# Kernel optimization log

Measured on AMD Instinct MI355X. Metric: run time of the kernel, lower is better.

## Reference

```python
import jax, jax.numpy as jnp
import numpy as np

DIM = 1024
NUM_HEADS = 16
HEAD_DIM = 64  # DIM // NUM_HEADS
BATCH = 2
SEQ = 2048


def setup_inputs() -> dict:
    key = jax.random.key(0)
    ks = jax.random.split(key, 6)
    x = jax.random.normal(ks[0], (BATCH, SEQ, DIM), dtype=jnp.float32)
    # Linear weights stored as [in, out] so y = x @ W (same math as torch Linear).
    Wq = jax.random.normal(ks[1], (DIM, DIM), dtype=jnp.float32) * (DIM ** -0.5)
    # MQA: single shared KV head of size HEAD_DIM.
    Wk = jax.random.normal(ks[2], (DIM, HEAD_DIM), dtype=jnp.float32) * (DIM ** -0.5)
    Wv = jax.random.normal(ks[3], (DIM, HEAD_DIM), dtype=jnp.float32) * (DIM ** -0.5)
    Wo = jax.random.normal(ks[4], (DIM, DIM), dtype=jnp.float32) * (DIM ** -0.5)
    bo = jax.random.normal(ks[5], (DIM,), dtype=jnp.float32) * 0.01
    return {"x": x, "Wq": Wq, "Wk": Wk, "Wv": Wv, "Wo": Wo, "bo": bo}


def reference(x, Wq, Wk, Wv, Wo, bo):
    b, s, _ = x.shape
    scale = HEAD_DIM ** -0.5
    # Per-head queries [b, h, s, d]
    q = (x @ Wq).reshape(b, s, NUM_HEADS, HEAD_DIM).transpose(0, 2, 1, 3) * scale
    # Shared single KV head [b, s, d]
    k = x @ Wk
    v = x @ Wv
    # Materialized scores [b, h, s_q, s_k]
    scores = jnp.einsum('bhqd,bkd->bhqk', q, k)
    causal = jnp.tril(jnp.ones((s, s), dtype=bool))  # True where allowed
    scores = jnp.where(causal, scores, -jnp.inf)
    # Manual stable softmax (max, exp, sum, div) as in the original
    max_scores = jnp.max(scores, axis=-1, keepdims=True)
    exp_scores = jnp.exp(scores - max_scores)
    attn = exp_scores / jnp.sum(exp_scores, axis=-1, keepdims=True)
    out = jnp.einsum('bhqk,bkd->bhqd', attn, v)  # [b, h, s, d]
    out = out.transpose(0, 2, 1, 3).reshape(b, s, DIM)
    return out @ Wo + bo
```

## Files before the change

### kernel.cpp

```cpp
#include <hip/hip_runtime.h>

typedef unsigned short u16;
typedef __attribute__((ext_vector_type(8))) short short8;
typedef __attribute__((ext_vector_type(4))) float f32x4;

static __device__ __forceinline__ u16 f32_to_bf16(float f) {
  unsigned u = __float_as_uint(f);
  u += 0x7fffu + ((u >> 16) & 1u);
  return (u16)(u >> 16);
}

static __device__ __forceinline__ void async16(u16* lds, const u16* g) {
  __builtin_amdgcn_global_load_lds(
      (const __attribute__((address_space(1))) void*)g,
      (__attribute__((address_space(3))) void*)lds, 16, 0, 0);
}


__global__ void __launch_bounds__(256) prep_kernel(
    const float* __restrict__ x,
    const float* __restrict__ Wq, const float* __restrict__ Wk,
    const float* __restrict__ Wv, const float* __restrict__ Wo,
    u16* __restrict__ Xb, u16* __restrict__ WqT, u16* __restrict__ WkvT,
    u16* __restrict__ WoT) {
  __shared__ u16 T[64][72];
  int id = blockIdx.x;
  int tid = threadIdx.x;
  if (id < 2048) {
    int base = (id * 256 + tid) * 8;
    float4 a = *(const float4*)&x[base];
    float4 b = *(const float4*)&x[base + 4];
    short8 v;
    v[0] = (short)f32_to_bf16(a.x); v[1] = (short)f32_to_bf16(a.y);
    v[2] = (short)f32_to_bf16(a.z); v[3] = (short)f32_to_bf16(a.w);
    v[4] = (short)f32_to_bf16(b.x); v[5] = (short)f32_to_bf16(b.y);
    v[6] = (short)f32_to_bf16(b.z); v[7] = (short)f32_to_bf16(b.w);
    *(short8*)&Xb[base] = v;
    return;
  }
  int id2 = id - 2048;
  const float* src; u16* dst; int tk, tn, src_ld, row_off;
  if (id2 < 256)      { src = Wq; dst = WqT;  tk = id2 & 15; tn = id2 >> 4; src_ld = 1024; row_off = 0; }
  else if (id2 < 512) { int i = id2 - 256; src = Wo; dst = WoT; tk = i & 15; tn = i >> 4; src_ld = 1024; row_off = 0; }
  else if (id2 < 528) { src = Wk; dst = WkvT; tk = id2 - 512; tn = 0; src_ld = 64; row_off = 0; }
  else                { src = Wv; dst = WkvT; tk = id2 - 528; tn = 0; src_ld = 64; row_off = 64; }
  int k0 = tk * 64, n0 = tn * 64;
#pragma unroll
  for (int it = 0; it < 2; ++it) {
    int c = tid + it * 256;
    int r = c >> 3, cc = (c & 7) * 8;
    const float* p = &src[(k0 + r) * src_ld + n0 + cc];
    float4 a = *(const float4*)&p[0];
    float4 b = *(const float4*)&p[4];
    short8 v;
    v[0] = (short)f32_to_bf16(a.x); v[1] = (short)f32_to_bf16(a.y);
    v[2] = (short)f32_to_bf16(a.z); v[3] = (short)f32_to_bf16(a.w);
    v[4] = (short)f32_to_bf16(b.x); v[5] = (short)f32_to_bf16(b.y);
    v[6] = (short)f32_to_bf16(b.z); v[7] = (short)f32_to_bf16(b.w);
    *(short8*)&T[r][cc] = v;
  }
  __syncthreads();
#pragma unroll
  for (int it = 0; it < 2; ++it) {
    int c = tid + it * 256;
    int r = c >> 3, cc = (c & 7) * 8;
    short8 v;
#pragma unroll
    for (int j = 0; j < 8; ++j) v[j] = (short)T[cc + j][r];
    *(short8*)&dst[(row_off + n0 + r) * 1024 + k0 + cc] = v;
  }
}

__device__ __forceinline__ void stage_64x128(
    const u16* __restrict__ A, const u16* __restrict__ BT, int m0, int K,
    int k0, u16* As, u16* Bs, int w, int lrow, int swz8) {
#pragma unroll
  for (int it = 0; it < 2; ++it) {
    int W = w * 2 + it;
    async16(As + W * 512, &A[(size_t)(m0 + W * 8 + lrow) * K + k0 + swz8]);
  }
#pragma unroll
  for (int it = 0; it < 4; ++it) {
    int W = w * 4 + it;
    async16(Bs + W * 512, &BT[(size_t)(W * 8 + lrow) * K + k0 + swz8]);
  }
}

__device__ __forceinline__ void gemm_core_64x128_db(
    const u16* __restrict__ A, const u16* __restrict__ BT, int m0, int K,
    f32x4 (&acc)[2][4], u16* As, u16* Bs,
    int lane, int w, int wr, int wc, int g, int lo) {
  int lrow = lane >> 3;
  int swz8 = ((lane & 7) ^ lrow) * 8;
  int lo7 = lo & 7;
  const int NK = K >> 6;
  stage_64x128(A, BT, m0, K, 0, As, Bs, w, lrow, swz8);
  for (int kt = 0; kt < NK; ++kt) {
    int cur = kt & 1;
    __syncthreads();
    if (kt + 1 < NK)
      stage_64x128(A, BT, m0, K, (kt + 1) * 64,
                   As + (cur ^ 1) * 4096, Bs + (cur ^ 1) * 8192, w, lrow, swz8);
    const u16* Asc = As + cur * 4096;
    const u16* Bsc = Bs + cur * 8192;
#pragma unroll
    for (int ks = 0; ks < 2; ++ks) {
      int pc = ((ks * 4 + g) ^ lo7) * 8;
      short8 af[2], bf[4];
#pragma unroll
      for (int i = 0; i < 2; ++i)
        af[i] = *(const short8*)&Asc[(wr * 32 + i * 16 + lo) * 64 + pc];
#pragma unroll
      for (int i = 0; i < 4; ++i)
        bf[i] = *(const short8*)&Bsc[(wc * 64 + i * 16 + lo) * 64 + pc];
#pragma unroll
      for (int mi = 0; mi < 2; ++mi)
#pragma unroll
        for (int ni = 0; ni < 4; ++ni)
          acc[mi][ni] = __builtin_amdgcn_mfma_f32_16x16x32_bf16(
              af[mi], bf[ni], acc[mi][ni], 0, 0, 0);
    }
  }
}

__global__ void __launch_bounds__(256) qkv_gemm(
    const u16* __restrict__ Xb, const u16* __restrict__ WqT,
    const u16* __restrict__ WkvT, u16* __restrict__ Qb, u16* __restrict__ KVb,
    u16* __restrict__ VTb) {
  __shared__ u16 As[2 * 64 * 64];
  __shared__ u16 Bs[2 * 128 * 64];
  int tid = threadIdx.x, lane = tid & 63, w = tid >> 6;
  int wr = w >> 1, wc = w & 1, g = lane >> 4, lo = lane & 15;
  int m0 = blockIdx.x * 64, nb = blockIdx.y;
  const u16* BT = (nb < 8) ? (WqT + (size_t)nb * 128 * 1024) : WkvT;
  f32x4 acc[2][4];
  f32x4 zz = {0.f, 0.f, 0.f, 0.f};
#pragma unroll
  for (int i = 0; i < 2; ++i)
#pragma unroll
    for (int j = 0; j < 4; ++j) acc[i][j] = zz;
  gemm_core_64x128_db(Xb, BT, m0, 1024, acc, As, Bs, lane, w, wr, wc, g, lo);
#pragma unroll
  for (int mi = 0; mi < 2; ++mi)
#pragma unroll
    for (int ni = 0; ni < 4; ++ni)
#pragma unroll
      for (int r = 0; r < 4; ++r) {
        int row = m0 + wr * 32 + mi * 16 + g * 4 + r;
        int col = wc * 64 + ni * 16 + lo;
        u16 v = f32_to_bf16(acc[mi][ni][r]);
        if (nb < 8) {
          Qb[row * 1024 + nb * 128 + col] = v;
        } else if (wc == 0) {
          KVb[row * 64 + col] = v;
        } else {
          int d = col - 64;
          VTb[(((row >> 11) * 64) + d) * 2048 + (row & 2047)] = v;
        }
      }
}

__global__ void __launch_bounds__(256, 2) attn_kernel(
    const u16* __restrict__ Qb, const u16* __restrict__ KVb,
    const u16* __restrict__ VTb, u16* __restrict__ AOb) {
  __shared__ u16 Ks[2][64 * 64];
  __shared__ u16 Vt[2][64 * 64];
  __shared__ u16 Ps[4][16][72];
  int tid = threadIdx.x, lane = tid & 63, w = tid >> 6;
  int gq = lane >> 4, lo = lane & 15;
  int pg = blockIdx.x;
  int h = blockIdx.y;
  int z = blockIdx.z;
  int b = z;
  int a = z ? (15 - pg) : pg;
  int hi = 31 - a;
  int qb_lo = a * 64 + w * 16;
  int qb_hi = hi * 64 + w * 16;
  int lrow = lane >> 3;
  int swz8 = ((lane & 7) ^ lrow) * 8;
  int lo7 = lo & 7;

  short8 qf_lo[2], qf_hi[2];
  {
    const u16* qp = &Qb[(size_t)(b * 2048 + qb_lo + lo) * 1024 + h * 64];
    qf_lo[0] = *(const short8*)&qp[gq * 8];
    qf_lo[1] = *(const short8*)&qp[32 + gq * 8];
    const u16* qp2 = &Qb[(size_t)(b * 2048 + qb_hi + lo) * 1024 + h * 64];
    qf_hi[0] = *(const short8*)&qp2[gq * 8];
    qf_hi[1] = *(const short8*)&qp2[32 + gq * 8];
  }

  short8 ones;
#pragma unroll
  for (int j = 0; j < 8; ++j) ones[j] = (short)0x3F80;

  f32x4 zz = {0.f, 0.f, 0.f, 0.f};
  f32x4 oacc_lo[4], oacc_hi[4], l_lo, l_hi;
#pragma unroll
  for (int i = 0; i < 4; ++i) { oacc_lo[i] = zz; oacc_hi[i] = zz; }
  l_lo = zz; l_hi = zz;

  const float kExp = 0.18033688011112042f;
  const float kOff = 11.541560327111707f;

  auto do_strip = [&](const short8 (&qf)[2], f32x4 (&oacc)[4], f32x4& l_acc,
                      int qbase, bool diag, int k0,
                      const u16* Kc, const u16* Vc) {
    f32x4 sacc[4];
#pragma unroll
    for (int ns = 0; ns < 4; ++ns) sacc[ns] = zz;
#pragma unroll
    for (int ks = 0; ks < 2; ++ks) {
      int pc = ((ks * 4 + gq) ^ lo7) * 8;
      short8 kf[4];
#pragma unroll
      for (int ns = 0; ns < 4; ++ns)
        kf[ns] = *(const short8*)&Kc[(ns * 16 + lo) * 64 + pc];
#pragma unroll
      for (int ns = 0; ns < 4; ++ns)
        sacc[ns] = __builtin_amdgcn_mfma_f32_16x16x32_bf16(
            qf[ks], kf[ns], sacc[ns], 0, 0, 0);
    }
#pragma unroll
    for (int ns = 0; ns < 4; ++ns)
#pragma unroll
      for (int r = 0; r < 4; ++r) {
        float p = __builtin_amdgcn_exp2f(fmaf(sacc[ns][r], kExp, -kOff));
        if (diag) {
          int qg = qbase + gq * 4 + r;
          int kg = k0 + ns * 16 + lo;
          if (kg > qg) p = 0.f;
        }
        Ps[w][gq * 4 + r][ns * 16 + lo] = (u16)(__float_as_uint(p) >> 16);
      }
    __threadfence_block();
#pragma unroll
    for (int k2 = 0; k2 < 2; ++k2) {
      short8 pf = *(const short8*)&Ps[w][lo][k2 * 32 + gq * 8];
      int pc = ((k2 * 4 + gq) ^ lo7) * 8;
      short8 vf[4];
#pragma unroll
      for (int ds = 0; ds < 4; ++ds)
        vf[ds] = *(const short8*)&Vc[(ds * 16 + lo) * 64 + pc];
#pragma unroll
      for (int ds = 0; ds < 4; ++ds)
        oacc[ds] = __builtin_amdgcn_mfma_f32_16x16x32_bf16(
            pf, vf[ds], oacc[ds], 0, 0, 0);
      l_acc = __builtin_amdgcn_mfma_f32_16x16x32_bf16(pf, ones, l_acc, 0, 0, 0);
    }
  };

  auto stage_kv = [&](int t, int bu) {
#pragma unroll
    for (int it = 0; it < 2; ++it) {
      int W = w * 2 + it;
      async16(&Ks[bu][W * 512],
              &KVb[(size_t)(b * 2048 + t * 64 + W * 8 + lrow) * 64 + swz8]);
      async16(&Vt[bu][W * 512],
              &VTb[((size_t)b * 64 + W * 8 + lrow) * 2048 + t * 64 + swz8]);
    }
  };

  int nst = hi + 1;
  stage_kv(0, 0);
  for (int t = 0; t < nst; ++t) {
    int cur = t & 1;
    __syncthreads();
    if (t + 1 < nst) stage_kv(t + 1, cur ^ 1);
    int k0 = t * 64;
    do_strip(qf_hi, oacc_hi, l_hi, qb_hi, t == hi, k0, Ks[cur], Vt[cur]);
    if (t <= a)
      do_strip(qf_lo, oacc_lo, l_lo, qb_lo, t == a, k0, Ks[cur], Vt[cur]);
  }

#pragma unroll
  for (int r = 0; r < 4; ++r) {
    float inv_lo = 1.0f / l_lo[r];
    float inv_hi = 1.0f / l_hi[r];
    int row_lo = b * 2048 + qb_lo + gq * 4 + r;
    int row_hi = b * 2048 + qb_hi + gq * 4 + r;
#pragma unroll
    for (int ds = 0; ds < 4; ++ds) {
      AOb[row_lo * 1024 + h * 64 + ds * 16 + lo] = f32_to_bf16(oacc_lo[ds][r] * inv_lo);
      AOb[row_hi * 1024 + h * 64 + ds * 16 + lo] = f32_to_bf16(oacc_hi[ds][r] * inv_hi);
    }
  }
}

__global__ void __launch_bounds__(256) out_gemm(
    const u16* __restrict__ A, const u16* __restrict__ WoT,
    const float* __restrict__ bias, float* __restrict__ C) {
  __shared__ u16 As[2 * 64 * 64];
  __shared__ u16 Bs[2 * 128 * 64];
  int tid = threadIdx.x, lane = tid & 63, w = tid >> 6;
  int wr = w >> 1, wc = w & 1, g = lane >> 4, lo = lane & 15;
  int m0 = blockIdx.x * 64, nb = blockIdx.y;
  const u16* BT = WoT + (size_t)nb * 128 * 1024;
  f32x4 acc[2][4];
  f32x4 zz = {0.f, 0.f, 0.f, 0.f};
#pragma unroll
  for (int i = 0; i < 2; ++i)
#pragma unroll
    for (int j = 0; j < 4; ++j) acc[i][j] = zz;
  gemm_core_64x128_db(A, BT, m0, 1024, acc, As, Bs, lane, w, wr, wc, g, lo);
#pragma unroll
  for (int mi = 0; mi < 2; ++mi)
#pragma unroll
    for (int ni = 0; ni < 4; ++ni)
#pragma unroll
      for (int r = 0; r < 4; ++r) {
        int row = m0 + wr * 32 + mi * 16 + g * 4 + r;
        int col = nb * 128 + wc * 64 + ni * 16 + lo;
        C[row * 1024 + col] = acc[mi][ni][r] + bias[col];
      }
}

extern "C" void kernel_launch(void* const* d_in, const int* in_sizes, int n_in,
                              void* d_out, int out_size, void* d_ws, size_t ws_size,
                              hipStream_t stream) {
  const float* x  = (const float*)d_in[0];
  const float* Wq = (const float*)d_in[1];
  const float* Wk = (const float*)d_in[2];
  const float* Wv = (const float*)d_in[3];
  const float* Wo = (const float*)d_in[4];
  const float* bo = (const float*)d_in[5];
  float* out = (float*)d_out;

  u16* ws   = (u16*)d_ws;
  u16* AOb  = ws;
  u16* KVb  = AOb + 4194304;
  u16* VTb  = KVb + 262144;
  u16* Xb   = VTb + 262144;
  u16* WqT  = Xb + 4194304;
  u16* WoT  = WqT + 1048576;
  u16* WkvT = WoT + 1048576;
  u16* Qb   = (u16*)d_out;

  prep_kernel<<<2592, 256, 0, stream>>>(x, Wq, Wk, Wv, Wo, Xb, WqT, WkvT, WoT);
  qkv_gemm<<<dim3(64, 9), 256, 0, stream>>>(Xb, WqT, WkvT, Qb, KVb, VTb);
  attn_kernel<<<dim3(16, 16, 2), 256, 0, stream>>>(Qb, KVb, VTb, AOb);
  out_gemm<<<dim3(64, 8), 256, 0, stream>>>(AOb, WoT, bo, out);
}
```

Baseline: 158.1 us.

## Restructure attention to one query tile per block with transposed MFMA and register row sums

The attention kernel drops the paired low/high query-tile scheme and instead launches one 64-row query tile per block, with a rotated block-to-tile mapping to spread causal work across the grid. The QK and PV MFMAs swap operand order so each lane holds a query column. The row sum is then accumulated in registers and reduced by shuffles, replacing the extra ones-matrix MFMA. P and the output are stored with packed bf16 conversion into a swizzled, unpadded LDS layout, and occupancy is raised to 4 blocks per SM. This removes the extra MFMA and lowers register pressure, but gives up the perfect load balance of pairing tiles and relies on the scheduler to absorb the uneven causal tile lengths.

```diff
diff --git a/kernel.cpp b/kernel.cpp
--- a/kernel.cpp
+++ b/kernel.cpp
@@ -8,6 +8,12 @@
   unsigned u = __float_as_uint(f);
   u += 0x7fffu + ((u >> 16) & 1u);
   return (u16)(u >> 16);
+}
+
+static __device__ __forceinline__ unsigned cvt_pk_bf16(float a, float b) {
+  unsigned r;
+  asm("v_cvt_pk_bf16_f32 %0, %1, %2" : "=v"(r) : "v"(a), "v"(b));
+  return r;
 }
 
 static __device__ __forceinline__ void async16(u16* lds, const u16* g) {
@@ -160,95 +166,37 @@
       }
 }
 
-__global__ void __launch_bounds__(256, 2) attn_kernel(
+__global__ void __launch_bounds__(256, 4) attn_kernel(
     const u16* __restrict__ Qb, const u16* __restrict__ KVb,
     const u16* __restrict__ VTb, u16* __restrict__ AOb) {
   __shared__ u16 Ks[2][64 * 64];
   __shared__ u16 Vt[2][64 * 64];
-  __shared__ u16 Ps[4][16][72];
+  __shared__ u16 Ps[4][16][64];
   int tid = threadIdx.x, lane = tid & 63, w = tid >> 6;
   int gq = lane >> 4, lo = lane & 15;
-  int pg = blockIdx.x;
   int h = blockIdx.y;
-  int z = blockIdx.z;
-  int b = z;
-  int a = z ? (15 - pg) : pg;
-  int hi = 31 - a;
-  int qb_lo = a * 64 + w * 16;
-  int qb_hi = hi * 64 + w * 16;
+  int b = blockIdx.z;
+  int a = (blockIdx.x + (h & 8) + (b << 4)) & 31;
+  int qb = a * 64 + w * 16;
   int lrow = lane >> 3;
   int swz8 = ((lane & 7) ^ lrow) * 8;
   int lo7 = lo & 7;
 
-  short8 qf_lo[2], qf_hi[2];
+  short8 qf[2];
   {
-    const u16* qp = &Qb[(size_t)(b * 2048 + qb_lo + lo) * 1024 + h * 64];
-    qf_lo[0] = *(const short8*)&qp[gq * 8];
-    qf_lo[1] = *(const short8*)&qp[32 + gq * 8];
-    const u16* qp2 = &Qb[(size_t)(b * 2048 + qb_hi + lo) * 1024 + h * 64];
-    qf_hi[0] = *(const short8*)&qp2[gq * 8];
-    qf_hi[1] = *(const short8*)&qp2[32 + gq * 8];
-  }
-
-  short8 ones;
-#pragma unroll
-  for (int j = 0; j < 8; ++j) ones[j] = (short)0x3F80;
+    const u16* qp = &Qb[(size_t)(b * 2048 + qb + lo) * 1024 + h * 64];
+    qf[0] = *(const short8*)&qp[gq * 8];
+    qf[1] = *(const short8*)&qp[32 + gq * 8];
+  }
 
   f32x4 zz = {0.f, 0.f, 0.f, 0.f};
-  f32x4 oacc_lo[4], oacc_hi[4], l_lo, l_hi;
-#pragma unroll
-  for (int i = 0; i < 4; ++i) { oacc_lo[i] = zz; oacc_hi[i] = zz; }
-  l_lo = zz; l_hi = zz;
+  f32x4 oacc[4];
+#pragma unroll
+  for (int i = 0; i < 4; ++i) oacc[i] = zz;
+  float lsum = 0.f;
 
   const float kExp = 0.18033688011112042f;
   const float kOff = 11.541560327111707f;
-
-  auto do_strip = [&](const short8 (&qf)[2], f32x4 (&oacc)[4], f32x4& l_acc,
-                      int qbase, bool diag, int k0,
-                      const u16* Kc, const u16* Vc) {
-    f32x4 sacc[4];
-#pragma unroll
-    for (int ns = 0; ns < 4; ++ns) sacc[ns] = zz;
-#pragma unroll
-    for (int ks = 0; ks < 2; ++ks) {
-      int pc = ((ks * 4 + gq) ^ lo7) * 8;
-      short8 kf[4];
-#pragma unroll
-      for (int ns = 0; ns < 4; ++ns)
-        kf[ns] = *(const short8*)&Kc[(ns * 16 + lo) * 64 + pc];
-#pragma unroll
-      for (int ns = 0; ns < 4; ++ns)
-        sacc[ns] = __builtin_amdgcn_mfma_f32_16x16x32_bf16(
-            qf[ks], kf[ns], sacc[ns], 0, 0, 0);
-    }
-#pragma unroll
-    for (int ns = 0; ns < 4; ++ns)
-#pragma unroll
-      for (int r = 0; r < 4; ++r) {
-        float p = __builtin_amdgcn_exp2f(fmaf(sacc[ns][r], kExp, -kOff));
-        if (diag) {
-          int qg = qbase + gq * 4 + r;
-          int kg = k0 + ns * 16 + lo;
-          if (kg > qg) p = 0.f;
-        }
-        Ps[w][gq * 4 + r][ns * 16 + lo] = (u16)(__float_as_uint(p) >> 16);
-      }
-    __threadfence_block();
-#pragma unroll
-    for (int k2 = 0; k2 < 2; ++k2) {
-      short8 pf = *(const short8*)&Ps[w][lo][k2 * 32 + gq * 8];
-      int pc = ((k2 * 4 + gq) ^ lo7) * 8;
-      short8 vf[4];
-#pragma unroll
-      for (int ds = 0; ds < 4; ++ds)
-        vf[ds] = *(const short8*)&Vc[(ds * 16 + lo) * 64 + pc];
-#pragma unroll
-      for (int ds = 0; ds < 4; ++ds)
-        oacc[ds] = __builtin_amdgcn_mfma_f32_16x16x32_bf16(
-            pf, vf[ds], oacc[ds], 0, 0, 0);
-      l_acc = __builtin_amdgcn_mfma_f32_16x16x32_bf16(pf, ones, l_acc, 0, 0, 0);
-    }
-  };
 
   auto stage_kv = [&](int t, int bu) {
 #pragma unroll
@@ -261,29 +209,79 @@
     }
   };
 
-  int nst = hi + 1;
+  int nst = a + 1;
   stage_kv(0, 0);
   for (int t = 0; t < nst; ++t) {
     int cur = t & 1;
     __syncthreads();
     if (t + 1 < nst) stage_kv(t + 1, cur ^ 1);
-    int k0 = t * 64;
-    do_strip(qf_hi, oacc_hi, l_hi, qb_hi, t == hi, k0, Ks[cur], Vt[cur]);
-    if (t <= a)
-      do_strip(qf_lo, oacc_lo, l_lo, qb_lo, t == a, k0, Ks[cur], Vt[cur]);
-  }
-
-#pragma unroll
-  for (int r = 0; r < 4; ++r) {
-    float inv_lo = 1.0f / l_lo[r];
-    float inv_hi = 1.0f / l_hi[r];
-    int row_lo = b * 2048 + qb_lo + gq * 4 + r;
-    int row_hi = b * 2048 + qb_hi + gq * 4 + r;
-#pragma unroll
-    for (int ds = 0; ds < 4; ++ds) {
-      AOb[row_lo * 1024 + h * 64 + ds * 16 + lo] = f32_to_bf16(oacc_lo[ds][r] * inv_lo);
-      AOb[row_hi * 1024 + h * 64 + ds * 16 + lo] = f32_to_bf16(oacc_hi[ds][r] * inv_hi);
-    }
+    const u16* Kc = Ks[cur];
+    const u16* Vc = Vt[cur];
+
+    f32x4 sacc[4];
+#pragma unroll
+    for (int ns = 0; ns < 4; ++ns) sacc[ns] = zz;
+#pragma unroll
+    for (int ks = 0; ks < 2; ++ks) {
+      int pc = ((ks * 4 + gq) ^ lo7) * 8;
+      short8 kf[4];
+#pragma unroll
+      for (int ns = 0; ns < 4; ++ns)
+        kf[ns] = *(const short8*)&Kc[(ns * 16 + lo) * 64 + pc];
+#pragma unroll
+      for (int ns = 0; ns < 4; ++ns)
+        sacc[ns] = __builtin_amdgcn_mfma_f32_16x16x32_bf16(
+            kf[ns], qf[ks], sacc[ns], 0, 0, 0);
+    }
+
+    bool diag = (t == a);
+    int qg = qb + lo;
+#pragma unroll
+    for (int ns = 0; ns < 4; ++ns) {
+      float p[4];
+#pragma unroll
+      for (int r = 0; r < 4; ++r) {
+        float pv = __builtin_amdgcn_exp2f(fmaf(sacc[ns][r], kExp, -kOff));
+        if (diag) {
+          int kg = t * 64 + ns * 16 + gq * 4 + r;
+          if (kg > qg) pv = 0.f;
+        }
+        lsum += pv;
+        p[r] = pv;
+      }
+      uint2 pd;
+      pd.x = cvt_pk_bf16(p[0], p[1]);
+      pd.y = cvt_pk_bf16(p[2], p[3]);
+      int ch = (2 * ns + (gq >> 1)) ^ lo7;
+      *(uint2*)&Ps[w][lo][ch * 8 + (gq & 1) * 4] = pd;
+    }
+    __threadfence_block();
+
+#pragma unroll
+    for (int k2 = 0; k2 < 2; ++k2) {
+      int pc = ((k2 * 4 + gq) ^ lo7) * 8;
+      short8 pf = *(const short8*)&Ps[w][lo][pc];
+      short8 vf[4];
+#pragma unroll
+      for (int ds = 0; ds < 4; ++ds)
+        vf[ds] = *(const short8*)&Vc[(ds * 16 + lo) * 64 + pc];
+#pragma unroll
+      for (int ds = 0; ds < 4; ++ds)
+        oacc[ds] = __builtin_amdgcn_mfma_f32_16x16x32_bf16(
+            vf[ds], pf, oacc[ds], 0, 0, 0);
+    }
+  }
+
+  lsum += __shfl_xor(lsum, 16);
+  lsum += __shfl_xor(lsum, 32);
+  float inv = 1.0f / lsum;
+  int row = b * 2048 + qb + lo;
+#pragma unroll
+  for (int ds = 0; ds < 4; ++ds) {
+    uint2 od;
+    od.x = cvt_pk_bf16(oacc[ds][0] * inv, oacc[ds][1] * inv);
+    od.y = cvt_pk_bf16(oacc[ds][2] * inv, oacc[ds][3] * inv);
+    *(uint2*)&AOb[(size_t)row * 1024 + h * 64 + ds * 16 + gq * 4] = od;
   }
 }
 
@@ -338,6 +336,6 @@
 
   prep_kernel<<<2592, 256, 0, stream>>>(x, Wq, Wk, Wv, Wo, Xb, WqT, WkvT, WoT);
   qkv_gemm<<<dim3(64, 9), 256, 0, stream>>>(Xb, WqT, WkvT, Qb, KVb, VTb);
-  attn_kernel<<<dim3(16, 16, 2), 256, 0, stream>>>(Qb, KVb, VTb, AOb);
+  attn_kernel<<<dim3(32, 16, 2), 256, 0, stream>>>(Qb, KVb, VTb, AOb);
   out_gemm<<<dim3(64, 8), 256, 0, stream>>>(AOb, WoT, bo, out);
 }
```

After: 156.2 us. About the same (-1.2%).
